# Performance work log

Hardware: AMD Instinct MI355X
Metric: run time of the kernel (lower is better)

## Reference

```python
import jax, jax.numpy as jnp
import numpy as np

N = 200000
E = 500000
F_IN = 165
HID = 256
N_CLASSES = 2


def setup_inputs() -> dict:
    key = jax.random.key(0)
    ks = jax.random.split(key, 8)
    x = jax.random.normal(ks[0], (N, F_IN), dtype=jnp.float32)
    edge_index = jax.random.randint(ks[1], (2, E), 0, N, dtype=jnp.int64)
    # PyG SAGEConv params: lin_l applied to mean-aggregated neighbors (with bias),
    # lin_r applied to root features (no bias). Glorot-ish init scale.
    def lin(k, fin, fout):
        return jax.random.normal(k, (fin, fout), dtype=jnp.float32) / np.sqrt(fin)
    return {
        "x": x,
        "edge_index": edge_index,
        "w1_l": lin(ks[2], F_IN, HID),
        "w1_r": lin(ks[3], F_IN, HID),
        "b1": jnp.zeros((HID,), dtype=jnp.float32),
        "w2_l": lin(ks[4], HID, N_CLASSES),
        "w2_r": lin(ks[5], HID, N_CLASSES),
        "b2": jnp.zeros((N_CLASSES,), dtype=jnp.float32),
    }


def _sage_conv(x, edge_index, w_l, w_r, b):
    # PyG SAGEConv with default mean aggregation:
    #   out = lin_l(mean_{j in N(i)} x_j) + lin_r(x_i) + b
    src, dst = edge_index[0], edge_index[1]
    n = x.shape[0]
    deg = jax.ops.segment_sum(jnp.ones((src.shape[0],), x.dtype), dst, num_segments=n)
    agg = jax.ops.segment_sum(x[src], dst, num_segments=n)  # [N, F]
    agg = agg / jnp.maximum(deg, 1.0)[:, None]
    return agg @ w_l + x @ w_r + b


def reference(x, edge_index, w1_l, w1_r, b1, w2_l, w2_r, b2):
    h = jax.nn.relu(_sage_conv(x, edge_index, w1_l, w1_r, b1))
    # F.dropout(training=self.training) is identity in eval mode.
    logits = _sage_conv(h, edge_index, w2_l, w2_r, b2)
    return (logits, edge_index)
```

## Files before the change

kernel.cpp:

```cpp
#include <hip/hip_runtime.h>
#include <hip/hip_bf16.h>
#include <hip/hip_fp16.h>

#define N_NODES 200000
#define N_EDGES 500000
#define F_IN    165
#define HID     256
#define SX      192
#define NB      782

typedef float    floatx4 __attribute__((ext_vector_type(4)));
typedef float    floatx4a __attribute__((ext_vector_type(4), aligned(16)));
typedef float    float4u __attribute__((ext_vector_type(4), aligned(4)));
typedef _Float16 half8   __attribute__((ext_vector_type(8)));

__global__ void cast_x_kernel(const float* __restrict__ x, half8* __restrict__ xh8) {
    int idx = blockIdx.x * blockDim.x + threadIdx.x;
    int row = idx / 24;
    int p = idx - row * 24;
    int f0 = p * 8;
    const float* px = x + (long)row * F_IN + f0;
    half8 r;
    if (f0 + 8 <= F_IN) {
        float4u lo = *(const float4u*)px;
        float4u hi = *(const float4u*)(px + 4);
#pragma unroll
        for (int q = 0; q < 4; ++q) r[q] = (_Float16)lo[q];
#pragma unroll
        for (int q = 0; q < 4; ++q) r[4 + q] = (_Float16)hi[q];
    } else {
#pragma unroll
        for (int q = 0; q < 8; ++q)
            r[q] = (f0 + q < F_IN) ? (_Float16)px[q] : (_Float16)0.0f;
    }
    xh8[idx] = r;
}

__global__ void hist_kernel(const int* __restrict__ ei, int* __restrict__ degi) {
    int e = blockIdx.x * blockDim.x + threadIdx.x;
    if (e < N_EDGES) atomicAdd(&degi[ei[N_EDGES + e]], 1);
}

__global__ __launch_bounds__(256) void block_sum_kernel(const int* __restrict__ degi,
                                                        int* __restrict__ bsum) {
    __shared__ int sh[256];
    int t = threadIdx.x, i = blockIdx.x * 256 + t;
    sh[t] = (i < N_NODES) ? degi[i] : 0;
    __syncthreads();
#pragma unroll
    for (int off = 128; off > 0; off >>= 1) {
        if (t < off) sh[t] += sh[t + off];
        __syncthreads();
    }
    if (t == 0) bsum[blockIdx.x] = sh[0];
}

__global__ __launch_bounds__(1024) void scan_bsum_kernel(const int* __restrict__ bsum,
                                                         int* __restrict__ boff,
                                                         int* __restrict__ row_start) {
    __shared__ int sh[1024];
    int t = threadIdx.x;
    int v = (t < NB) ? bsum[t] : 0;
    sh[t] = v;
    __syncthreads();
    for (int off = 1; off < 1024; off <<= 1) {
        int u = (t >= off) ? sh[t - off] : 0;
        __syncthreads();
        sh[t] += u;
        __syncthreads();
    }
    if (t < NB) boff[t] = sh[t] - v;
    if (t == 1023) row_start[N_NODES] = sh[1023];
}

__global__ __launch_bounds__(256) void scan_emit_kernel(const int* __restrict__ degi,
                                                        const int* __restrict__ boff,
                                                        int* __restrict__ row_start,
                                                        int* __restrict__ cursor,
                                                        float* __restrict__ invdeg) {
    __shared__ int sh[256];
    int t = threadIdx.x, i = blockIdx.x * 256 + t;
    int d = (i < N_NODES) ? degi[i] : 0;
    sh[t] = d;
    __syncthreads();
#pragma unroll
    for (int off = 1; off < 256; off <<= 1) {
        int u = (t >= off) ? sh[t - off] : 0;
        __syncthreads();
        sh[t] += u;
        __syncthreads();
    }
    if (i < N_NODES) {
        int row = boff[blockIdx.x] + sh[t] - d;
        row_start[i] = row;
        cursor[i] = row;
        invdeg[i] = 1.0f / fmaxf((float)d, 1.0f);
    }
}

__global__ void scatter_edges_kernel(const int* __restrict__ ei,
                                     int* __restrict__ cursor,
                                     int* __restrict__ csr) {
    int e = blockIdx.x * blockDim.x + threadIdx.x;
    if (e >= N_EDGES) return;
    int s = ei[e];
    int d = ei[N_EDGES + e];
    int pos = atomicAdd(&cursor[d], 1);
    csr[pos] = s;
}

__global__ void gather_agg_kernel(const half8* __restrict__ xh8,
                                  const int* __restrict__ row_start,
                                  const int* __restrict__ csr,
                                  half8* __restrict__ aggh8) {
    int idx = blockIdx.x * blockDim.x + threadIdx.x;
    int n = idx / 24;
    int p = idx - n * 24;
    int e0 = row_start[n], e1 = row_start[n + 1];
    half8 acc = {0, 0, 0, 0, 0, 0, 0, 0};
    half8 acc2 = {0, 0, 0, 0, 0, 0, 0, 0};
    int e = e0;
    for (; e + 2 <= e1; e += 2) {
        int s0 = csr[e], s1 = csr[e + 1];
        half8 v0 = xh8[(long)s0 * 24 + p];
        half8 v1 = xh8[(long)s1 * 24 + p];
        acc += v0;
        acc2 += v1;
    }
    if (e < e1) acc += xh8[(long)csr[e] * 24 + p];
    aggh8[idx] = acc + acc2;
}

__global__ void prep_bfrag_kernel(const float* __restrict__ w1l,
                                  const float* __restrict__ w1r,
                                  _Float16* __restrict__ bfrag) {
    int gid = blockIdx.x * blockDim.x + threadIdx.x;
    if (gid >= 12 * 16 * 64) return;
    int lane = gid & 63;
    int j = (gid >> 6) & 15;
    int c = gid >> 10;
    int quad = lane >> 4, n = lane & 15;
    const float* w = (c < 6) ? w1l : w1r;
    int kb = (c < 6 ? c : c - 6) * 32;
    int col = j * 16 + n;
    half8 r;
#pragma unroll
    for (int q = 0; q < 8; ++q) {
        int k = kb + quad * 8 + q;
        r[q] = (_Float16)((k < F_IN) ? w[k * HID + col] : 0.0f);
    }
    *(half8*)(bfrag + gid * 8) = r;
}

__global__ __launch_bounds__(512, 2) void gemm_fused_kernel(
        const _Float16* __restrict__ xh, const _Float16* __restrict__ aggh,
        const float* __restrict__ invdeg, const _Float16* __restrict__ bfrag,
        const float* __restrict__ b1,
        const float* __restrict__ w2l, const float* __restrict__ w2r,
        float* __restrict__ tl, float* __restrict__ tr) {
    __shared__ __attribute__((aligned(16))) _Float16 As[2][128 * 32];
    __shared__ float tlr[128][4];
    const int tid = threadIdx.x;
    const int w = tid >> 6, lane = tid & 63;
    const int quad = lane >> 4, l15 = lane & 15;
    const int rowbase = blockIdx.x * 128;
    const int mrow0 = rowbase + (w & 1) * 64;
    const int rhalf = (w & 1) * 64;
    const int jbase = (w >> 1) * 4;

    ((float*)tlr)[tid < 512 ? tid : 0] = 0.0f;

    const int srow_l = tid >> 2;
    const int sseg = (tid & 3) ^ ((srow_l >> 1) & 3);
    int srow = rowbase + srow_l;
    if (srow >= N_NODES) srow = N_NODES - 1;
    const long sgoff = (long)srow * SX + sseg * 8;

    floatx4 acc[4][4];
#pragma unroll
    for (int i = 0; i < 4; ++i)
#pragma unroll
        for (int jj = 0; jj < 4; ++jj)
            acc[i][jj] = (floatx4){0.f, 0.f, 0.f, 0.f};

    __syncthreads();

#pragma unroll 1
    for (int it = 0; it < 6; ++it) {
#pragma unroll
        for (int u = 0; u < 2; ++u) {
            const int cc = it * 2 + u;
            const _Float16* __restrict__ src = (cc < 6) ? aggh : xh;
            const int kb = (cc < 6 ? cc : cc - 6) * 32;
            const _Float16* gp = src + sgoff + kb;
            char* dst = (char*)(&As[u][0]) + (tid & ~63) * 16;
            __builtin_amdgcn_global_load_lds(
                (const __attribute__((address_space(1))) void*)gp,
                (__attribute__((address_space(3))) void*)dst, 16, 0, 0);
        }
        __syncthreads();

#pragma unroll
        for (int u = 0; u < 2; ++u) {
            const int cc = it * 2 + u;
            half8 a[4], b[4];
#pragma unroll
            for (int i = 0; i < 4; ++i) {
                int r = rhalf + i * 16 + l15;
                int slot = r * 4 + (quad ^ ((r >> 1) & 3));
                a[i] = *(const half8*)(&As[u][slot * 8]);
            }
#pragma unroll
            for (int jj = 0; jj < 4; ++jj)
                b[jj] = *(const half8*)(bfrag + (((cc * 16) + jbase + jj) * 64 + lane) * 8);
#pragma unroll
            for (int i = 0; i < 4; ++i)
#pragma unroll
                for (int jj = 0; jj < 4; ++jj)
                    acc[i][jj] = __builtin_amdgcn_mfma_f32_16x16x32_f16(a[i], b[jj], acc[i][jj], 0, 0, 0);

            if (cc == 5) {
#pragma unroll
                for (int i = 0; i < 4; ++i) {
                    int rb = mrow0 + i * 16 + quad * 4;
                    floatx4 iv;
                    if (rb + 3 < N_NODES) {
                        iv = *(const floatx4a*)(invdeg + rb);
                    } else {
#pragma unroll
                        for (int t = 0; t < 4; ++t)
                            iv[t] = (rb + t < N_NODES) ? invdeg[rb + t] : 0.0f;
                    }
#pragma unroll
                    for (int jj = 0; jj < 4; ++jj)
                        acc[i][jj] *= iv;
                }
            }
        }
        __syncthreads();
    }

    float bb[4], wl0[4], wl1[4], wr0[4], wr1[4];
#pragma unroll
    for (int jj = 0; jj < 4; ++jj) {
        int col = (w >> 1) * 64 + jj * 16 + l15;
        bb[jj]  = b1[col];
        wl0[jj] = w2l[col * 2];  wl1[jj] = w2l[col * 2 + 1];
        wr0[jj] = w2r[col * 2];  wr1[jj] = w2r[col * 2 + 1];
    }
#pragma unroll
    for (int i = 0; i < 4; ++i) {
#pragma unroll
        for (int t = 0; t < 4; ++t) {
            float s0 = 0.f, s1 = 0.f, s2 = 0.f, s3 = 0.f;
#pragma unroll
            for (int jj = 0; jj < 4; ++jj) {
                float v = fmaxf(acc[i][jj][t] + bb[jj], 0.0f);
                s0 += v * wl0[jj]; s1 += v * wl1[jj];
                s2 += v * wr0[jj]; s3 += v * wr1[jj];
            }
#pragma unroll
            for (int m = 1; m < 16; m <<= 1) {
                s0 += __shfl_xor(s0, m, 64);
                s1 += __shfl_xor(s1, m, 64);
                s2 += __shfl_xor(s2, m, 64);
                s3 += __shfl_xor(s3, m, 64);
            }
            if (l15 == 0) {
                int rl = (w & 1) * 64 + i * 16 + quad * 4 + t;
                atomicAdd(&tlr[rl][0], s0);
                atomicAdd(&tlr[rl][1], s1);
                atomicAdd(&tlr[rl][2], s2);
                atomicAdd(&tlr[rl][3], s3);
            }
        }
    }
    __syncthreads();
    if (tid < 128) {
        int row = rowbase + tid;
        if (row < N_NODES) {
            tl[row * 2 + 0] = tlr[tid][0];
            tl[row * 2 + 1] = tlr[tid][1];
            tr[row * 2 + 0] = tlr[tid][2];
            tr[row * 2 + 1] = tlr[tid][3];
        }
    }
}

__global__ void gather_out_kernel(const int* __restrict__ row_start,
                                  const int* __restrict__ csr,
                                  const float* __restrict__ tl,
                                  const float* __restrict__ tr,
                                  const float* __restrict__ invdeg,
                                  const float* __restrict__ b2,
                                  float* __restrict__ out) {
    int i = blockIdx.x * blockDim.x + threadIdx.x;
    if (i >= N_NODES) return;
    int e0 = row_start[i], e1 = row_start[i + 1];
    float a0 = 0.f, a1 = 0.f;
    for (int e = e0; e < e1; ++e) {
        int s = csr[e];
        a0 += tl[s * 2 + 0];
        a1 += tl[s * 2 + 1];
    }
    float inv = invdeg[i];
    out[i * 2 + 0] = a0 * inv + tr[i * 2 + 0] + b2[0];
    out[i * 2 + 1] = a1 * inv + tr[i * 2 + 1] + b2[1];
}

__global__ void cast_edges_kernel(const int* __restrict__ ei,
                                  float* __restrict__ out) {
    int i = blockIdx.x * blockDim.x + threadIdx.x;
    if (i < 2 * N_EDGES) out[i] = (float)ei[i];
}

extern "C" void kernel_launch(void* const* d_in, const int* in_sizes, int n_in,
                              void* d_out, int out_size, void* d_ws, size_t ws_size,
                              hipStream_t stream) {
    const float* x    = (const float*)d_in[0];
    const int*   ei   = (const int*)d_in[1];
    const float* w1_l = (const float*)d_in[2];
    const float* w1_r = (const float*)d_in[3];
    const float* b1   = (const float*)d_in[4];
    const float* w2_l = (const float*)d_in[5];
    const float* w2_r = (const float*)d_in[6];
    const float* b2   = (const float*)d_in[7];

    char* ws = (char*)d_ws;
    int*   degi      = (int*)(ws);
    int*   row_start = (int*)(ws + 800000);
    int*   cursor    = (int*)(ws + 1600032);
    float* invdeg    = (float*)(ws + 2400032);
    int*   csr       = (int*)(ws + 3200032);
    float* tl        = (float*)(ws + 5200032);
    float* tr        = (float*)(ws + 6800032);
    int*   bsum      = (int*)(ws + 8400032);
    int*   boff      = (int*)(ws + 8403232);
    _Float16* bfrag  = (_Float16*)(ws + 8406432);
    _Float16* aggh   = (_Float16*)(ws + 8610000);
    _Float16* xh     = (_Float16*)(ws + 85410000);

    float* out = (float*)d_out;

    (void)hipMemsetAsync(degi, 0, 800000, stream);

    cast_x_kernel<<<(N_NODES * 24) / 256, 256, 0, stream>>>(x, (half8*)xh);
    prep_bfrag_kernel<<<48, 256, 0, stream>>>(w1_l, w1_r, bfrag);

    hist_kernel<<<(N_EDGES + 255) / 256, 256, 0, stream>>>(ei, degi);
    block_sum_kernel<<<NB, 256, 0, stream>>>(degi, bsum);
    scan_bsum_kernel<<<1, 1024, 0, stream>>>(bsum, boff, row_start);
    scan_emit_kernel<<<NB, 256, 0, stream>>>(degi, boff, row_start, cursor, invdeg);
    scatter_edges_kernel<<<(N_EDGES + 255) / 256, 256, 0, stream>>>(ei, cursor, csr);

    gather_agg_kernel<<<(N_NODES * 24) / 256, 256, 0, stream>>>(
        (const half8*)xh, row_start, csr, (half8*)aggh);

    gemm_fused_kernel<<<(N_NODES + 127) / 128, 512, 0, stream>>>(
        xh, aggh, invdeg, bfrag, b1, w2_l, w2_r, tl, tr);

    gather_out_kernel<<<NB, 256, 0, stream>>>(row_start, csr, tl, tr, invdeg, b2, out);
    cast_edges_kernel<<<(2 * N_EDGES + 255) / 256, 256, 0, stream>>>(ei, out + 2 * N_NODES);
}
```

Before: 424.8 us.

## Double-buffer LDS tiles in fused GEMM to overlap loads with MFMA

Converts the fused layer-1 GEMM loop to a double-buffered pipeline: the next pair of K-chunks is prefetched into an alternate LDS buffer while MFMAs run on the current one, with one barrier per iteration instead of two. It also precomputes LDS and B-fragment byte offsets, switches to 32-bit global offsets, and raises the launch-bounds occupancy hint from 2 to 4 blocks. LDS use per block doubles, and the stricter occupancy hint may force register spilling given the 64-float accumulator array.

```diff
diff --git a/kernel.cpp b/kernel.cpp
--- a/kernel.cpp
+++ b/kernel.cpp
@@ -152,13 +152,13 @@
     *(half8*)(bfrag + gid * 8) = r;
 }
 
-__global__ __launch_bounds__(512, 2) void gemm_fused_kernel(
+__global__ __launch_bounds__(512, 4) void gemm_fused_kernel(
         const _Float16* __restrict__ xh, const _Float16* __restrict__ aggh,
         const float* __restrict__ invdeg, const _Float16* __restrict__ bfrag,
         const float* __restrict__ b1,
         const float* __restrict__ w2l, const float* __restrict__ w2r,
         float* __restrict__ tl, float* __restrict__ tr) {
-    __shared__ __attribute__((aligned(16))) _Float16 As[2][128 * 32];
+    __shared__ __attribute__((aligned(16))) _Float16 As[2][128 * 64];
     __shared__ float tlr[128][4];
     const int tid = threadIdx.x;
     const int w = tid >> 6, lane = tid & 63;
@@ -168,13 +168,23 @@
     const int rhalf = (w & 1) * 64;
     const int jbase = (w >> 1) * 4;
 
-    ((float*)tlr)[tid < 512 ? tid : 0] = 0.0f;
+    ((float*)tlr)[tid] = 0.0f;
 
     const int srow_l = tid >> 2;
     const int sseg = (tid & 3) ^ ((srow_l >> 1) & 3);
     int srow = rowbase + srow_l;
     if (srow >= N_NODES) srow = N_NODES - 1;
-    const long sgoff = (long)srow * SX + sseg * 8;
+    const int sgoff = srow * SX + sseg * 8;
+    const int ldst = (tid & ~63) * 16;
+
+    int aoff[4];
+#pragma unroll
+    for (int i = 0; i < 4; ++i) {
+        int r = rhalf + i * 16 + l15;
+        int slot = r * 4 + (quad ^ ((r >> 1) & 3));
+        aoff[i] = slot * 16;
+    }
+    const int boff = (jbase * 64 + lane) * 16;
 
     floatx4 acc[4][4];
 #pragma unroll
@@ -183,61 +193,65 @@
         for (int jj = 0; jj < 4; ++jj)
             acc[i][jj] = (floatx4){0.f, 0.f, 0.f, 0.f};
 
-    __syncthreads();
-
-#pragma unroll 1
-    for (int it = 0; it < 6; ++it) {
+    auto STAGE = [&](int p) {
 #pragma unroll
         for (int u = 0; u < 2; ++u) {
-            const int cc = it * 2 + u;
-            const _Float16* __restrict__ src = (cc < 6) ? aggh : xh;
+            const int cc = 2 * p + u;
+            const _Float16* src = (cc < 6) ? aggh : xh;
             const int kb = (cc < 6 ? cc : cc - 6) * 32;
             const _Float16* gp = src + sgoff + kb;
-            char* dst = (char*)(&As[u][0]) + (tid & ~63) * 16;
+            char* dst = (char*)(&As[p & 1][u * 128 * 32]) + ldst;
             __builtin_amdgcn_global_load_lds(
                 (const __attribute__((address_space(1))) void*)gp,
                 (__attribute__((address_space(3))) void*)dst, 16, 0, 0);
         }
-        __syncthreads();
-
+    };
+
+    STAGE(0);
+    asm volatile("s_waitcnt vmcnt(0)" ::: "memory");
+    __builtin_amdgcn_s_barrier();
+    __builtin_amdgcn_sched_barrier(0);
+
+#pragma unroll 1
+    for (int t = 0; t < 6; ++t) {
+        if (t < 5) STAGE(t + 1);
+        const char* abase = (const char*)(&As[t & 1][0]);
 #pragma unroll
         for (int u = 0; u < 2; ++u) {
-            const int cc = it * 2 + u;
+            const int cc = 2 * t + u;
             half8 a[4], b[4];
 #pragma unroll
-            for (int i = 0; i < 4; ++i) {
-                int r = rhalf + i * 16 + l15;
-                int slot = r * 4 + (quad ^ ((r >> 1) & 3));
-                a[i] = *(const half8*)(&As[u][slot * 8]);
-            }
+            for (int i = 0; i < 4; ++i)
+                a[i] = *(const half8*)(abase + u * 8192 + aoff[i]);
 #pragma unroll
             for (int jj = 0; jj < 4; ++jj)
-                b[jj] = *(const half8*)(bfrag + (((cc * 16) + jbase + jj) * 64 + lane) * 8);
+                b[jj] = *(const half8*)((const char*)bfrag + boff + (cc * 16 + jj) * 1024);
 #pragma unroll
             for (int i = 0; i < 4; ++i)
 #pragma unroll
                 for (int jj = 0; jj < 4; ++jj)
                     acc[i][jj] = __builtin_amdgcn_mfma_f32_16x16x32_f16(a[i], b[jj], acc[i][jj], 0, 0, 0);
-
-            if (cc == 5) {
-#pragma unroll
-                for (int i = 0; i < 4; ++i) {
-                    int rb = mrow0 + i * 16 + quad * 4;
-                    floatx4 iv;
-                    if (rb + 3 < N_NODES) {
-                        iv = *(const floatx4a*)(invdeg + rb);
-                    } else {
-#pragma unroll
-                        for (int t = 0; t < 4; ++t)
-                            iv[t] = (rb + t < N_NODES) ? invdeg[rb + t] : 0.0f;
-                    }
-#pragma unroll
-                    for (int jj = 0; jj < 4; ++jj)
-                        acc[i][jj] *= iv;
+        }
+        if (t == 2) {
+#pragma unroll
+            for (int i = 0; i < 4; ++i) {
+                int rb = mrow0 + i * 16 + quad * 4;
+                floatx4 iv;
+                if (rb + 3 < N_NODES) {
+                    iv = *(const floatx4a*)(invdeg + rb);
+                } else {
+#pragma unroll
+                    for (int q = 0; q < 4; ++q)
+                        iv[q] = (rb + q < N_NODES) ? invdeg[rb + q] : 0.0f;
                 }
+#pragma unroll
+                for (int jj = 0; jj < 4; ++jj)
+                    acc[i][jj] *= iv;
             }
         }
-        __syncthreads();
+        asm volatile("s_waitcnt vmcnt(0)" ::: "memory");
+        __builtin_amdgcn_s_barrier();
+        __builtin_amdgcn_sched_barrier(0);
     }
 
     float bb[4], wl0[4], wl1[4], wr0[4], wr1[4];
@@ -251,11 +265,11 @@
 #pragma unroll
     for (int i = 0; i < 4; ++i) {
 #pragma unroll
-        for (int t = 0; t < 4; ++t) {
+        for (int q = 0; q < 4; ++q) {
             float s0 = 0.f, s1 = 0.f, s2 = 0.f, s3 = 0.f;
 #pragma unroll
             for (int jj = 0; jj < 4; ++jj) {
-                float v = fmaxf(acc[i][jj][t] + bb[jj], 0.0f);
+                float v = fmaxf(acc[i][jj][q] + bb[jj], 0.0f);
                 s0 += v * wl0[jj]; s1 += v * wl1[jj];
                 s2 += v * wr0[jj]; s3 += v * wr1[jj];
             }
@@ -267,7 +281,7 @@
                 s3 += __shfl_xor(s3, m, 64);
             }
             if (l15 == 0) {
-                int rl = (w & 1) * 64 + i * 16 + quad * 4 + t;
+                int rl = (w & 1) * 64 + i * 16 + quad * 4 + q;
                 atomicAdd(&tlr[rl][0], s0);
                 atomicAdd(&tlr[rl][1], s1);
                 atomicAdd(&tlr[rl][2], s2);
```

New measurement: 425.5 us. About the same (+0.2%).
